# Kernel tuning notes

Measured on AMD Instinct MI355X. Metric: run time of the kernel, lower is better.

Reference implementation:

```python
import jax, jax.numpy as jnp
import numpy as np
import math

D_MODEL = 128
N_HEAD = 8
D_K = D_MODEL // N_HEAD
NEG_INF = -1e30


def setup_inputs() -> dict:
    key = jax.random.key(0)
    ks = jax.random.split(key, 8)
    B, N, D = 4, 2048, D_MODEL
    s = 1.0 / math.sqrt(D)
    x = jax.random.normal(ks[0], (B, D, N), dtype=jnp.float32)
    mask = jnp.ones((B, N), dtype=jnp.float32)
    Wq = jax.random.normal(ks[1], (D, D), dtype=jnp.float32) * s
    Wk = jax.random.normal(ks[2], (D, D), dtype=jnp.float32) * s
    Wv = jax.random.normal(ks[3], (D, D), dtype=jnp.float32) * s
    Wfc = jax.random.normal(ks[4], (D, D), dtype=jnp.float32) * s
    z = jnp.zeros((D,), dtype=jnp.float32)
    return {"x": x, "mask": mask, "Wq": Wq, "bq": z, "Wk": Wk, "bk": z,
            "Wv": Wv, "bv": z, "Wfc": Wfc, "bfc": z}


def reference(x, mask, Wq, bq, Wk, bk, Wv, bv, Wfc, bfc):
    # x: [B, D, N], mask: [B, N]
    B, D, N = x.shape
    xt = jnp.swapaxes(x, 1, 2)  # [B, N, D]
    q = (xt @ Wq.T + bq).reshape(B, N, N_HEAD, D_K)
    k = (xt @ Wk.T + bk).reshape(B, N, N_HEAD, D_K)
    v = (xt @ Wv.T + bv).reshape(B, N, N_HEAD, D_K)
    # scores: [B, H, Nq, Nk]; NOTE: original scales by sqrt(d_model), not sqrt(d_k)
    scores = jnp.einsum('bnhd,bmhd->bhnm', q, k) / jnp.sqrt(jnp.float32(D))
    # multiplicative mask_logits over the key dimension
    m = mask[:, None, None, :]  # [B, 1, 1, Nk]
    scores = scores * m + (1.0 - m) * NEG_INF
    atten = jax.nn.softmax(scores, axis=-1)  # dropout is identity (p=0 / eval)
    out = jnp.einsum('bhnm,bmhd->bnhd', atten, v).reshape(B, N, D)
    out = out @ Wfc.T + bfc
    return jnp.swapaxes(out, 1, 2)  # [B, D, N]
```

## Files before the change

kernel.cpp:

```cpp
#include <hip/hip_runtime.h>
#include <stdint.h>

#define BSZ  4
#define NSEQ 2048
#define DM   128
#define NH   8
#define DK   16
#define LOG2E 1.4426950408889634f
#define SCALE_QL 0.1275156338341935f
#define W_SCALE 3.814697265625e-6f

typedef __bf16          bf16x8v __attribute__((ext_vector_type(8)));
typedef float           f32x4   __attribute__((ext_vector_type(4)));
typedef float           f32x16  __attribute__((ext_vector_type(16)));
typedef unsigned short  u16x8   __attribute__((ext_vector_type(8)));
typedef unsigned short  u16x4   __attribute__((ext_vector_type(4)));
typedef unsigned int    u32x2   __attribute__((ext_vector_type(2)));
typedef unsigned int    u32x4   __attribute__((ext_vector_type(4)));

__device__ __forceinline__ unsigned short f2bf(float f) {
    unsigned u = __float_as_uint(f);
    u = (u + 0x7fffu + ((u >> 16) & 1u)) >> 16;
    return (unsigned short)u;
}

__device__ __forceinline__ unsigned int pack2bf(float a, float b) {
#if __has_builtin(__builtin_amdgcn_cvt_pk_bf16_f32)
    typedef __bf16 bf16x2 __attribute__((ext_vector_type(2)));
    bf16x2 v = __builtin_amdgcn_cvt_pk_bf16_f32(a, b);
    return __builtin_bit_cast(unsigned int, v);
#else
    return (unsigned)f2bf(a) | ((unsigned)f2bf(b) << 16);
#endif
}

__device__ __forceinline__ float exp2_(float x) {
#if __has_builtin(__builtin_amdgcn_exp2f)
    return __builtin_amdgcn_exp2f(x);
#else
    return exp2f(x);
#endif
}

__device__ __forceinline__ u16x8 cvt8(const float* p, float sc) {
    const f32x4 a = *reinterpret_cast<const f32x4*>(p);
    const f32x4 b = *reinterpret_cast<const f32x4*>(p + 4);
    u32x4 u = {pack2bf(a[0] * sc, a[1] * sc), pack2bf(a[2] * sc, a[3] * sc),
               pack2bf(b[0] * sc, b[1] * sc), pack2bf(b[2] * sc, b[3] * sc)};
    return __builtin_bit_cast(u16x8, u);
}

__device__ __forceinline__ f32x4 mfma16(u16x8 a, u16x8 b, f32x4 c) {
    return __builtin_amdgcn_mfma_f32_16x16x32_bf16(
        __builtin_bit_cast(bf16x8v, a), __builtin_bit_cast(bf16x8v, b), c, 0, 0, 0);
}
__device__ __forceinline__ f32x16 mfma32(u16x8 a, u16x8 b, f32x16 c) {
    return __builtin_amdgcn_mfma_f32_32x32x16_bf16(
        __builtin_bit_cast(bf16x8v, a), __builtin_bit_cast(bf16x8v, b), c, 0, 0, 0);
}

__global__ __launch_bounds__(768) void k_qkv(
    const float* __restrict__ x,
    const float* __restrict__ Wq, const float* __restrict__ bq,
    const float* __restrict__ Wk, const float* __restrict__ bk,
    const float* __restrict__ Wv, const float* __restrict__ bv,
    const float* __restrict__ Wfc, const float* __restrict__ mask,
    unsigned short* __restrict__ Q, unsigned short* __restrict__ Kb,
    unsigned short* __restrict__ Vt,
    unsigned short* __restrict__ WfcB, unsigned short* __restrict__ wb)
{
    __shared__ __align__(16) float xs[DM * 36];
    const int tid = threadIdx.x;

    const int gt = blockIdx.x * 768 + tid;
    if (gt < DM * DM) {
        WfcB[gt] = f2bf(Wfc[gt]);
    } else if (gt < DM * DM + BSZ * NSEQ) {
        const int i = gt - DM * DM;
        wb[i] = f2bf(mask[i] * W_SCALE);
    }

    const int b  = blockIdx.x >> 6;
    const int n0 = (blockIdx.x & 63) << 5;

#pragma unroll
    for (int i = tid; i < 1024; i += 768) {
        const int d = i >> 3, c4 = (i & 7) << 2;
        *reinterpret_cast<f32x4*>(&xs[d * 36 + c4]) =
            *reinterpret_cast<const f32x4*>(x + (size_t)(b * DM + d) * NSEQ + n0 + c4);
    }
    __syncthreads();

    const int lane = tid & 63;
    const int wv   = tid >> 6;
    const int mat  = wv >> 2;
    const int nt   = (wv >> 1) & 1;
    const int th   = wv & 1;
    const int c    = lane & 15;
    const int quad = lane >> 4;
    const int col  = n0 + nt * 16 + c;

    u16x8 xf[4];
#pragma unroll
    for (int kk = 0; kk < 4; ++kk) {
        float f[8];
#pragma unroll
        for (int j = 0; j < 8; ++j)
            f[j] = xs[(kk * 32 + quad * 8 + j) * 36 + nt * 16 + c];
        u32x4 u = {pack2bf(f[0], f[1]), pack2bf(f[2], f[3]),
                   pack2bf(f[4], f[5]), pack2bf(f[6], f[7])};
        xf[kk] = __builtin_bit_cast(u16x8, u);
    }

    const float* W    = (mat == 0) ? Wq : (mat == 1) ? Wk : Wv;
    const float* bias = (mat == 0) ? bq : (mat == 1) ? bk : bv;
    const float  sc   = (mat == 0) ? SCALE_QL : 1.0f;
    const float  vw   = (mat == 2) ? mask[b * NSEQ + col] * W_SCALE : 0.f;

#pragma unroll
    for (int tt = 0; tt < 4; ++tt) {
        const int t = th * 4 + tt;
        f32x4 acc = {0.f, 0.f, 0.f, 0.f};
#pragma unroll
        for (int kk = 0; kk < 4; ++kk)
            acc = mfma16(cvt8(W + (t * 16 + c) * DM + kk * 32 + quad * 8, sc),
                         xf[kk], acc);
        if (mat == 2) {
#pragma unroll
            for (int r = 0; r < 4; ++r)
                Vt[((b * NH + t) * DK + quad * 4 + r) * NSEQ + col] =
                    f2bf((acc[r] + bias[t * 16 + quad * 4 + r]) * vw);
        } else {
            u16x4 pk;
#pragma unroll
            for (int r = 0; r < 4; ++r)
                pk[r] = f2bf(acc[r] + bias[t * 16 + quad * 4 + r] * sc);
            *reinterpret_cast<u16x4*>(
                (mat == 0 ? Q : Kb) + ((size_t)(b * NH + t) * NSEQ + col) * DK +
                quad * 4) = pk;
        }
    }
}

__global__ __launch_bounds__(256, 4) void k_attn(
    const unsigned short* __restrict__ Q,
    const unsigned short* __restrict__ Kb,
    const unsigned short* __restrict__ Vt,
    const unsigned short* __restrict__ wb,
    unsigned short* __restrict__ AO)
{
    __shared__ __align__(16) char smem[17408];
    const int tid  = threadIdx.x;
    const int lane = tid & 63;
    const int w    = tid >> 6;
    const int q32  = lane & 31;
    const int c    = lane & 15;
    const int quad = lane >> 4;
    const int hi   = lane >> 5;

    const int b  = blockIdx.x >> 9;
    const int h  = (blockIdx.x >> 6) & 7;
    const int n0 = (blockIdx.x & 63) << 5;
    const int bh = b * NH + h;

    const u16x8 uq = *reinterpret_cast<const u16x8*>(
        Q + ((size_t)bh * NSEQ + n0 + q32) * DK + 8 * hi);

    const unsigned short* Kp = Kb + (size_t)bh * NSEQ * DK + 8 * hi;
    const unsigned short* Vp = Vt + ((size_t)bh * DK + c) * NSEQ + 8 * quad;
    const unsigned short* wp = wb + b * NSEQ + 8 * quad;

    char* pbase = smem + w * 4352;
    char* wrow  = pbase + q32 * 136 + 8 * hi;
    const char* rrow0 = pbase + c * 136 + 16 * quad;
    const char* rrow1 = pbase + (c + 16) * 136 + 16 * quad;

    f32x4 o0 = {0.f, 0.f, 0.f, 0.f}, o1 = {0.f, 0.f, 0.f, 0.f};
    f32x4 l0 = {0.f, 0.f, 0.f, 0.f}, l1 = {0.f, 0.f, 0.f, 0.f};
    const f32x16 z16 = {};
    const int kvb = w * (NSEQ / 4);

    u16x8 nk0 = *reinterpret_cast<const u16x8*>(Kp + (size_t)(kvb + q32) * DK);
    u16x8 nk1 = *reinterpret_cast<const u16x8*>(Kp + (size_t)(kvb + 32 + q32) * DK);

    for (int it = 0; it < 8; ++it) {
        const int kv0 = kvb + it * 64;
        const u16x8 uk0 = nk0, uk1 = nk1;
        if (it < 7) {
            nk0 = *reinterpret_cast<const u16x8*>(Kp + (size_t)(kv0 + 64 + q32) * DK);
            nk1 = *reinterpret_cast<const u16x8*>(Kp + (size_t)(kv0 + 96 + q32) * DK);
        }
        f32x16 S0 = mfma32(uk0, uq, z16);
        f32x16 S1 = mfma32(uk1, uq, z16);

#pragma unroll
        for (int i = 0; i < 16; ++i) {
            S0[i] = exp2_(S0[i]);
            S1[i] = exp2_(S1[i]);
        }

#pragma unroll
        for (int g = 0; g < 4; ++g) {
            u32x2 d0 = {pack2bf(S0[4 * g], S0[4 * g + 1]),
                        pack2bf(S0[4 * g + 2], S0[4 * g + 3])};
            u32x2 d1 = {pack2bf(S1[4 * g], S1[4 * g + 1]),
                        pack2bf(S1[4 * g + 2], S1[4 * g + 3])};
            *reinterpret_cast<u32x2*>(wrow + 16 * g) = d0;
            *reinterpret_cast<u32x2*>(wrow + 64 + 16 * g) = d1;
        }

#pragma unroll
        for (int t = 0; t < 2; ++t) {
            const u16x8 uv  = *reinterpret_cast<const u16x8*>(Vp + kv0 + 32 * t);
            const u16x8 uw  = *reinterpret_cast<const u16x8*>(wp + kv0 + 32 * t);
            const u16x8 up0 = *reinterpret_cast<const u16x8*>(rrow0 + 64 * t);
            const u16x8 up1 = *reinterpret_cast<const u16x8*>(rrow1 + 64 * t);
            o0 = mfma16(uv, up0, o0);
            o1 = mfma16(uv, up1, o1);
            l0 = mfma16(uw, up0, l0);
            l1 = mfma16(uw, up1, l1);
        }
    }

    __syncthreads();
    float* Lsm = reinterpret_cast<float*>(smem);
    float* Osm = reinterpret_cast<float*>(smem + 512);
    Lsm[w * 32 + c]      = l0[0];
    Lsm[w * 32 + 16 + c] = l1[0];
    *reinterpret_cast<f32x4*>(Osm + w * 640 + c * 20 + 4 * quad)        = o0;
    *reinterpret_cast<f32x4*>(Osm + w * 640 + (c + 16) * 20 + 4 * quad) = o1;
    __syncthreads();

    const int q   = tid >> 3;
    const int dk2 = (tid & 7) * 2;
    const float l = Lsm[q] + Lsm[32 + q] + Lsm[64 + q] + Lsm[96 + q];
    const float* Oq = Osm + q * 20 + dk2;
    const float v0 = Oq[0] + Oq[640] + Oq[1280] + Oq[1920];
    const float v1 = Oq[1] + Oq[641] + Oq[1281] + Oq[1921];
    const float inv = 1.0f / l;
    *reinterpret_cast<unsigned int*>(
        AO + ((size_t)(b * NSEQ) + n0 + q) * DM + h * DK + dk2) =
        pack2bf(v0 * inv, v1 * inv);
}

__global__ __launch_bounds__(256) void k_fc(
    const unsigned short* __restrict__ AO,
    const unsigned short* __restrict__ WfcB, const float* __restrict__ bfc,
    float* __restrict__ out)
{
    const int lane = threadIdx.x & 63;
    const int w    = threadIdx.x >> 6;
    const int c    = lane & 15;
    const int quad = lane >> 4;
    const int b    = blockIdx.x >> 8;
    const int n0   = ((blockIdx.x >> 1) & 127) << 4;
    const int t    = (blockIdx.x & 1) * 4 + w;

    u16x8 af[4];
#pragma unroll
    for (int kk = 0; kk < 4; ++kk)
        af[kk] = *reinterpret_cast<const u16x8*>(
            AO + ((size_t)(b * NSEQ) + n0 + c) * DM + kk * 32 + quad * 8);

    f32x4 acc = {0.f, 0.f, 0.f, 0.f};
#pragma unroll
    for (int kk = 0; kk < 4; ++kk)
        acc = mfma16(*reinterpret_cast<const u16x8*>(
                         WfcB + (t * 16 + c) * DM + kk * 32 + quad * 8),
                     af[kk], acc);
#pragma unroll
    for (int r = 0; r < 4; ++r)
        out[(size_t)(b * DM + t * 16 + quad * 4 + r) * NSEQ + n0 + c] =
            acc[r] + bfc[t * 16 + quad * 4 + r];
}

extern "C" void kernel_launch(void* const* d_in, const int* in_sizes, int n_in,
                              void* d_out, int out_size, void* d_ws, size_t ws_size,
                              hipStream_t stream)
{
    const float* x    = (const float*)d_in[0];
    const float* mask = (const float*)d_in[1];
    const float* Wq   = (const float*)d_in[2];
    const float* bq   = (const float*)d_in[3];
    const float* Wk   = (const float*)d_in[4];
    const float* bk   = (const float*)d_in[5];
    const float* Wv   = (const float*)d_in[6];
    const float* bv   = (const float*)d_in[7];
    const float* Wfc  = (const float*)d_in[8];
    const float* bfc  = (const float*)d_in[9];
    float* out = (float*)d_out;

    const size_t QKV_ELEMS = (size_t)BSZ * NH * NSEQ * DK;
    unsigned short* Q    = (unsigned short*)d_ws;
    unsigned short* Kb   = Q + QKV_ELEMS;
    unsigned short* Vt   = Kb + QKV_ELEMS;
    unsigned short* AO   = Vt + QKV_ELEMS;
    unsigned short* WfcB = AO + QKV_ELEMS;
    unsigned short* wb   = WfcB + DM * DM;

    k_qkv<<<256, 768, 0, stream>>>(x, Wq, bq, Wk, bk, Wv, bv, Wfc, mask,
                                   Q, Kb, Vt, WfcB, wb);
    k_attn<<<2048, 256, 0, stream>>>(Q, Kb, Vt, wb, AO);
    k_fc<<<1024, 256, 0, stream>>>(AO, WfcB, bfc, out);
}
```

Baseline: 132.6 us.

## Software-pipeline attention loop with double-buffered P tiles and MFMA priority hints

Restructures the attention inner loop so each iteration first reads the current P tile from LDS, then computes the next block's QK scores, exponentials and packed P writes into a second LDS buffer, and finally runs the PV and row-sum MFMAs. The goal is to overlap exp/pack/LDS-store work with the PV MFMAs and hide LDS and global load latency. s_setprio hints are added around MFMA groups. Per-block LDS doubles, which can lower occupancy at the 4-blocks-per-CU launch bound, and register pressure rises.

```diff
diff --git a/kernel.cpp b/kernel.cpp
--- a/kernel.cpp
+++ b/kernel.cpp
@@ -149,7 +149,7 @@
     const unsigned short* __restrict__ wb,
     unsigned short* __restrict__ AO)
 {
-    __shared__ __align__(16) char smem[17408];
+    __shared__ __align__(16) char smem[34816];
     const int tid  = threadIdx.x;
     const int lane = tid & 63;
     const int w    = tid >> 6;
@@ -170,10 +170,11 @@
     const unsigned short* Vp = Vt + ((size_t)bh * DK + c) * NSEQ + 8 * quad;
     const unsigned short* wp = wb + b * NSEQ + 8 * quad;
 
-    char* pbase = smem + w * 4352;
-    char* wrow  = pbase + q32 * 136 + 8 * hi;
-    const char* rrow0 = pbase + c * 136 + 16 * quad;
-    const char* rrow1 = pbase + (c + 16) * 136 + 16 * quad;
+    char* pbA = smem + w * 8704;
+    char* pbB = pbA + 4352;
+    const int wroff  = q32 * 136 + 8 * hi;
+    const int rd0off = c * 136 + 16 * quad;
+    const int rd1off = (c + 16) * 136 + 16 * quad;
 
     f32x4 o0 = {0.f, 0.f, 0.f, 0.f}, o1 = {0.f, 0.f, 0.f, 0.f};
     f32x4 l0 = {0.f, 0.f, 0.f, 0.f}, l1 = {0.f, 0.f, 0.f, 0.f};
@@ -183,22 +184,22 @@
     u16x8 nk0 = *reinterpret_cast<const u16x8*>(Kp + (size_t)(kvb + q32) * DK);
     u16x8 nk1 = *reinterpret_cast<const u16x8*>(Kp + (size_t)(kvb + 32 + q32) * DK);
 
-    for (int it = 0; it < 8; ++it) {
+    auto stage = [&](const int it, char* pb) {
         const int kv0 = kvb + it * 64;
-        const u16x8 uk0 = nk0, uk1 = nk1;
+        __builtin_amdgcn_s_setprio(1);
+        f32x16 S0 = mfma32(nk0, uq, z16);
+        f32x16 S1 = mfma32(nk1, uq, z16);
+        __builtin_amdgcn_s_setprio(0);
         if (it < 7) {
             nk0 = *reinterpret_cast<const u16x8*>(Kp + (size_t)(kv0 + 64 + q32) * DK);
             nk1 = *reinterpret_cast<const u16x8*>(Kp + (size_t)(kv0 + 96 + q32) * DK);
         }
-        f32x16 S0 = mfma32(uk0, uq, z16);
-        f32x16 S1 = mfma32(uk1, uq, z16);
-
 #pragma unroll
         for (int i = 0; i < 16; ++i) {
             S0[i] = exp2_(S0[i]);
             S1[i] = exp2_(S1[i]);
         }
-
+        char* wrow = pb + wroff;
 #pragma unroll
         for (int g = 0; g < 4; ++g) {
             u32x2 d0 = {pack2bf(S0[4 * g], S0[4 * g + 1]),
@@ -208,18 +209,40 @@
             *reinterpret_cast<u32x2*>(wrow + 16 * g) = d0;
             *reinterpret_cast<u32x2*>(wrow + 64 + 16 * g) = d1;
         }
-
-#pragma unroll
-        for (int t = 0; t < 2; ++t) {
-            const u16x8 uv  = *reinterpret_cast<const u16x8*>(Vp + kv0 + 32 * t);
-            const u16x8 uw  = *reinterpret_cast<const u16x8*>(wp + kv0 + 32 * t);
-            const u16x8 up0 = *reinterpret_cast<const u16x8*>(rrow0 + 64 * t);
-            const u16x8 up1 = *reinterpret_cast<const u16x8*>(rrow1 + 64 * t);
-            o0 = mfma16(uv, up0, o0);
-            o1 = mfma16(uv, up1, o1);
-            l0 = mfma16(uw, up0, l0);
-            l1 = mfma16(uw, up1, l1);
-        }
+    };
+
+    stage(0, pbA);
+
+#pragma unroll 2
+    for (int it = 0; it < 8; ++it) {
+        const int kv0 = kvb + it * 64;
+        char* pbc = (it & 1) ? pbB : pbA;
+        char* pbn = (it & 1) ? pbA : pbB;
+
+        const char* ra = pbc + rd0off;
+        const char* rb = pbc + rd1off;
+        const u16x8 up0a = *reinterpret_cast<const u16x8*>(ra);
+        const u16x8 up1a = *reinterpret_cast<const u16x8*>(rb);
+        const u16x8 up0b = *reinterpret_cast<const u16x8*>(ra + 64);
+        const u16x8 up1b = *reinterpret_cast<const u16x8*>(rb + 64);
+        const u16x8 uv0 = *reinterpret_cast<const u16x8*>(Vp + kv0);
+        const u16x8 uv1 = *reinterpret_cast<const u16x8*>(Vp + kv0 + 32);
+
+        if (it < 7) stage(it + 1, pbn);
+
+        const u16x8 uw0 = *reinterpret_cast<const u16x8*>(wp + kv0);
+        const u16x8 uw1 = *reinterpret_cast<const u16x8*>(wp + kv0 + 32);
+
+        __builtin_amdgcn_s_setprio(1);
+        o0 = mfma16(uv0, up0a, o0);
+        o1 = mfma16(uv0, up1a, o1);
+        l0 = mfma16(uw0, up0a, l0);
+        l1 = mfma16(uw0, up1a, l1);
+        o0 = mfma16(uv1, up0b, o0);
+        o1 = mfma16(uv1, up1b, o1);
+        l0 = mfma16(uw1, up0b, l0);
+        l1 = mfma16(uw1, up1b, l1);
+        __builtin_amdgcn_s_setprio(0);
     }
 
     __syncthreads();
```

After: 131.7 us. Within noise of the previous version (-0.7%).
